# Kernel optimization log

Hardware: AMD Instinct MI355X
Metric: run time of the kernel (lower is better)

## Reference

```python
import jax, jax.numpy as jnp
import numpy as np

EPS = 1e-8


def setup_inputs() -> dict:
    key = jax.random.key(0)
    ks = jax.random.split(key, 4)
    B, Cin, Cout, K, S, H, W = 16, 256, 256, 3, 512, 128, 128
    return {
        "x": jax.random.normal(ks[0], (B, Cin, H, W), dtype=jnp.float32),
        "style": jax.random.normal(ks[1], (B, S), dtype=jnp.float32),
        "weight": jax.random.normal(ks[2], (1, Cout, Cin, K, K), dtype=jnp.float32),
        "mod_w": jax.random.normal(ks[3], (Cin, S), dtype=jnp.float32) * (1.0 / np.sqrt(S)),
        "mod_b": jnp.zeros((Cin,), dtype=jnp.float32),
        "bias": jnp.zeros((1, Cout, 1, 1), dtype=jnp.float32),
    }


def reference(x, style, weight, mod_w, mod_b, bias):
    B, Cin, H, W = x.shape
    _, Cout, _, K, _ = weight.shape
    scale = 1.0 / np.sqrt(Cin * K * K)

    # modulation: Linear(style_dim -> in_channel)
    s = style @ mod_w.T + mod_b                      # [B, Cin]
    w = scale * weight * s[:, None, :, None, None]   # [B, Cout, Cin, K, K]
    demod = jax.lax.rsqrt(jnp.sum(w * w, axis=(2, 3, 4)) + EPS)  # [B, Cout]
    w = w * demod[:, :, None, None, None]

    # grouped conv with groups = batch (per-sample weights)
    w = w.reshape(B * Cout, Cin, K, K)
    xg = x.reshape(1, B * Cin, H, W)
    out = jax.lax.conv_general_dilated(
        xg, w,
        window_strides=(1, 1),
        padding=[(1, 1), (1, 1)],
        dimension_numbers=("NCHW", "OIHW", "NCHW"),
        feature_group_count=B,
    )
    Ho, Wo = out.shape[2], out.shape[3]
    out = out.reshape(B, Cout, Ho, Wo)
    return out + bias
```

## Files before the change

### kernel.cpp

```cpp
#include <hip/hip_runtime.h>
#include <stdint.h>

typedef unsigned short u16;
typedef __attribute__((ext_vector_type(8))) short short8;
typedef __attribute__((ext_vector_type(4))) float f32x4;

#define AS1 __attribute__((address_space(1)))
#define AS3 __attribute__((address_space(3)))

static __device__ __forceinline__ void gload_lds16(const void* g, void* l) {
  __builtin_amdgcn_global_load_lds((const AS1 void*)g, (AS3 void*)l, 16, 0, 0);
}

static __device__ __forceinline__ u16 bf16r(float f) {
  union { float f; uint32_t u; } c; c.f = f;
  uint32_t u = c.u;
  u += 0x7fffu + ((u >> 16) & 1u);
  return (u16)(u >> 16);
}

static constexpr int NB = 16, CIN = 256, COUT = 256, HW = 128, SDIM = 512;
static constexpr float SCALE = 1.0f / 48.0f;

__global__ void k_style(const float* __restrict__ style, const float* __restrict__ mod_w,
                        const float* __restrict__ mod_b, float* __restrict__ s) {
  int b = blockIdx.x, ci = threadIdx.x;
  const float4* st = (const float4*)(style + (size_t)b * SDIM);
  const float4* mw = (const float4*)(mod_w + (size_t)ci * SDIM);
  float acc = 0.f;
  #pragma unroll 4
  for (int j = 0; j < SDIM / 4; ++j) {
    float4 a = st[j], w = mw[j];
    acc += a.x * w.x + a.y * w.y + a.z * w.z + a.w * w.w;
  }
  s[b * CIN + ci] = acc + mod_b[ci];
}

__global__ void k_wmod(const float* __restrict__ weight, const float* __restrict__ s,
                       u16* __restrict__ Wb) {
  __shared__ float wld[CIN * 9];
  __shared__ float red[8];
  int bid = blockIdx.x;
  int b = bid >> 8, co = bid & 255;
  int t = threadIdx.x;
  const float* wsrc = weight + (size_t)co * (CIN * 9);
  for (int i = t; i < CIN * 9; i += 256) wld[i] = wsrc[i];
  __syncthreads();
  int ci = t;
  float sv = s[b * CIN + ci];
  float v[9];
  float sq = 0.f;
  #pragma unroll
  for (int k = 0; k < 9; ++k) {
    float w = SCALE * wld[ci * 9 + k] * sv;
    v[k] = w;
    sq += w * w;
  }
  #pragma unroll
  for (int off = 32; off; off >>= 1) sq += __shfl_down(sq, off);
  int lane = t & 63, wid = t >> 6;
  if (lane == 0) red[wid] = sq;
  __syncthreads();
  if (t == 0) red[4] = rsqrtf(red[0] + red[1] + red[2] + red[3] + 1e-8f);
  __syncthreads();
  float demod = red[4];
  #pragma unroll
  for (int k = 0; k < 9; ++k) {
    Wb[(((size_t)b * 9 + k) * COUT + co) * CIN + ci] = bf16r(v[k] * demod);
  }
}

__global__ void k_xt(const float* __restrict__ x, u16* __restrict__ xTp) {
  __shared__ u16 T[128 * 65];
  int bid = blockIdx.x;
  int b = bid >> 7, h = bid & 127;
  int t = threadIdx.x;
  size_t rowbase = ((size_t)b * 130 + (h + 1)) * 130 * CIN;
  xTp[rowbase + t] = 0;
  xTp[rowbase + (size_t)129 * CIN + t] = 0;
  if (h == 0) {
    uint32_t* g = (uint32_t*)(xTp + (size_t)b * 130 * 130 * CIN);
    for (int i = t; i < 130 * CIN / 2; i += 256) g[i] = 0;
  }
  if (h == 127) {
    uint32_t* g = (uint32_t*)(xTp + ((size_t)b * 130 + 129) * 130 * CIN);
    for (int i = t; i < 130 * CIN / 2; i += 256) g[i] = 0;
  }
  for (int ci0 = 0; ci0 < CIN; ci0 += 64) {
    __syncthreads();
    #pragma unroll
    for (int i = 0; i < 8; ++i) {
      int idx = t + i * 256;
      int ci = idx >> 5, px4 = idx & 31;
      float4 v = *(const float4*)(x + (((size_t)b * CIN + ci0 + ci) * HW + h) * HW + px4 * 4);
      T[(px4 * 4 + 0) * 65 + ci] = bf16r(v.x);
      T[(px4 * 4 + 1) * 65 + ci] = bf16r(v.y);
      T[(px4 * 4 + 2) * 65 + ci] = bf16r(v.z);
      T[(px4 * 4 + 3) * 65 + ci] = bf16r(v.w);
    }
    __syncthreads();
    int ci = t & 63, pxo = t >> 6;
    #pragma unroll
    for (int i = 0; i < 32; ++i) {
      int px = i * 4 + pxo;
      xTp[rowbase + (size_t)(px + 1) * CIN + ci0 + ci] = T[px * 65 + ci];
    }
  }
}

static constexpr int SLOTU = 32768;

__global__ __launch_bounds__(512, 2) void k_conv(const u16* __restrict__ Wb,
                                                 const u16* __restrict__ xTp,
                                                 const float* __restrict__ bias,
                                                 float* __restrict__ out) {
  extern __shared__ u16 lds[];
  int bid = blockIdx.x;
  int swz = (bid & 7) * 128 + (bid >> 3);
  int b = swz >> 6, hp = swz & 63;
  int h0 = hp * 2;

  int t = threadIdx.x, lane = t & 63, wid = t >> 6;
  int wr = wid >> 2, wc = wid & 3;
  int rowoff = wid * 8 + (lane >> 3);
  int swzc = ((lane & 7) ^ (lane >> 3)) << 3;
  int cxor = (lane & 7) << 3;
  int klo = (lane >> 4) << 3;
  int arow = (wr * 128 + (lane & 15)) * 64;
  int brow = (wc * 64 + (lane & 15)) * 64;
  const size_t wbB = (size_t)b * 9 * 65536;
  const size_t xB = (size_t)b * 130 * 130 * 256;

  f32x4 acc[8][4];
  #pragma unroll
  for (int i = 0; i < 8; ++i)
    #pragma unroll
    for (int j = 0; j < 4; ++j) acc[i][j] = (f32x4)0.f;

  auto srcA = [&](int kta, int i) -> const u16* {
    int kpos = kta >> 2, ci0 = (kta & 3) << 6;
    return Wb + wbB + (size_t)kpos * 65536 + (size_t)(i * 64 + rowoff) * 256 + ci0 + swzc;
  };
  auto srcB = [&](int kta, int i) -> const u16* {
    int kpos = kta >> 2, ci0 = (kta & 3) << 6;
    int kh = kpos < 3 ? 0 : (kpos < 6 ? 1 : 2);
    int kw = kpos - kh * 3;
    int hh = h0 + kh + (i >> 1);
    int pxp = kw + (i & 1) * 64 + rowoff;
    return xTp + xB + ((size_t)hh * 130 + pxp) * 256 + ci0 + swzc;
  };

  {
    u16* A2 = lds;
    u16* B2 = lds + 16384;
    #pragma unroll
    for (int i = 0; i < 4; ++i) gload_lds16(srcA(0, i), A2 + (i * 64 + wid * 8) * 64);
    #pragma unroll
    for (int i = 0; i < 4; ++i) gload_lds16(srcB(0, i), B2 + (i * 64 + wid * 8) * 64);
  }
  __syncthreads();

  for (int kt = 0; kt < 36; ++kt) {
    u16* Ac = lds + (kt & 1) * SLOTU;
    u16* Bc = Ac + 16384;
    u16* An = lds + ((kt & 1) ^ 1) * SLOTU;
    u16* Bn = An + 16384;
    bool pf = kt < 35;
    int kta = kt + 1;

#define LD_A(M, KK) (*(const short8*)&Ac[arow + (M) * 1024 + (((KK) * 32 + klo) ^ cxor)])
#define LD_B(N, KK) (*(const short8*)&Bc[brow + (N) * 1024 + (((KK) * 32 + klo) ^ cxor)])

    short8 af0[8], bf0[4], af1[8], bf1[4];
    #pragma unroll
    for (int mt = 0; mt < 8; ++mt) af0[mt] = LD_A(mt, 0);
    #pragma unroll
    for (int nt = 0; nt < 4; ++nt) bf0[nt] = LD_B(nt, 0);
    if (pf) {
      #pragma unroll
      for (int i = 0; i < 4; ++i) gload_lds16(srcA(kta, i), An + (i * 64 + wid * 8) * 64);
    }
    #pragma unroll
    for (int nt = 0; nt < 4; ++nt) bf1[nt] = LD_B(nt, 1);
    #pragma unroll
    for (int mt = 0; mt < 8; ++mt)
      #pragma unroll
      for (int nt = 0; nt < 4; ++nt)
        acc[mt][nt] = __builtin_amdgcn_mfma_f32_16x16x32_bf16(af0[mt], bf0[nt], acc[mt][nt], 0, 0, 0);
    if (pf) {
      #pragma unroll
      for (int i = 0; i < 4; ++i) gload_lds16(srcB(kta, i), Bn + (i * 64 + wid * 8) * 64);
    }
    #pragma unroll
    for (int mt = 0; mt < 8; ++mt) af1[mt] = LD_A(mt, 1);
    #pragma unroll
    for (int mt = 0; mt < 8; ++mt)
      #pragma unroll
      for (int nt = 0; nt < 4; ++nt)
        acc[mt][nt] = __builtin_amdgcn_mfma_f32_16x16x32_bf16(af1[mt], bf1[nt], acc[mt][nt], 0, 0, 0);
    __syncthreads();
#undef LD_A
#undef LD_B
  }

  #pragma unroll
  for (int mt = 0; mt < 8; ++mt) {
    #pragma unroll
    for (int j = 0; j < 4; ++j) {
      int co = wr * 128 + mt * 16 + ((lane >> 4) * 4) + j;
      float bv = bias[co];
      #pragma unroll
      for (int nt = 0; nt < 4; ++nt) {
        int px = wc * 64 + nt * 16 + (lane & 15);
        int h = h0 + (px >> 7), w = px & 127;
        out[(((size_t)b * COUT + co) * HW + h) * HW + w] = acc[mt][nt][j] + bv;
      }
    }
  }
}

extern "C" void kernel_launch(void* const* d_in, const int* in_sizes, int n_in,
                              void* d_out, int out_size, void* d_ws, size_t ws_size,
                              hipStream_t stream) {
  const float* x      = (const float*)d_in[0];
  const float* style  = (const float*)d_in[1];
  const float* weight = (const float*)d_in[2];
  const float* mod_w  = (const float*)d_in[3];
  const float* mod_b  = (const float*)d_in[4];
  const float* bias   = (const float*)d_in[5];
  float* out = (float*)d_out;

  char* ws = (char*)d_ws;
  float* s   = (float*)ws;
  u16* Wb    = (u16*)(ws + 16384);
  u16* xTp   = (u16*)(ws + 16384 + (size_t)NB * 9 * COUT * CIN * 2);

  (void)hipFuncSetAttribute((const void*)k_conv,
                            hipFuncAttributeMaxDynamicSharedMemorySize, 2 * SLOTU * 2);

  k_style<<<NB, 256, 0, stream>>>(style, mod_w, mod_b, s);
  k_wmod<<<NB * COUT, 256, 0, stream>>>(weight, s, Wb);
  k_xt<<<NB * HW, 256, 0, stream>>>(x, xTp);
  k_conv<<<NB * (HW / 2), 512, 2 * SLOTU * 2, stream>>>(Wb, xTp, bias, out);
}
```

Baseline: 408.8 us.

## Restructure conv mainloop into fine-grained staged prefetch with split barriers and setprio

Rewrites the k_conv main loop so global-to-LDS loads for the next one and two k-steps are issued in smaller per-half-K chunks between MFMA phases. Explicit vmcnt waits and raw s_barriers replace the single __syncthreads per step. The LDS layout becomes 32-element-wide half-K slabs with a new XOR swizzle, and s_setprio raises priority around MFMA bursts. The aim is to overlap memory traffic with matrix math and cut LDS bank conflicts, at the cost of more barriers and a tricky wait-count schedule that could race if the counts are off.

```diff
diff --git a/kernel.cpp b/kernel.cpp
--- a/kernel.cpp
+++ b/kernel.cpp
@@ -122,12 +122,12 @@
 
   int t = threadIdx.x, lane = t & 63, wid = t >> 6;
   int wr = wid >> 2, wc = wid & 3;
-  int rowoff = wid * 8 + (lane >> 3);
-  int swzc = ((lane & 7) ^ (lane >> 3)) << 3;
-  int cxor = (lane & 7) << 3;
-  int klo = (lane >> 4) << 3;
-  int arow = (wr * 128 + (lane & 15)) * 64;
-  int brow = (wc * 64 + (lane & 15)) * 64;
+  int l15 = lane & 15;
+  int sa8 = (((lane >> 4) ^ ((lane >> 1) & 3))) * 8;
+  int aro = (wr * 128 + l15) * 32 + sa8;
+  int bro = 16384 + (wc * 64 + l15) * 32 + sa8;
+  int srow = t >> 2;
+  int ssrc8 = ((t & 3) ^ ((t >> 3) & 3)) * 8;
   const size_t wbB = (size_t)b * 9 * 65536;
   const size_t xB = (size_t)b * 130 * 130 * 256;
 
@@ -137,68 +137,99 @@
     #pragma unroll
     for (int j = 0; j < 4; ++j) acc[i][j] = (f32x4)0.f;
 
-  auto srcA = [&](int kta, int i) -> const u16* {
+  auto srcA = [&](int kta, int kk, int i) -> const u16* {
     int kpos = kta >> 2, ci0 = (kta & 3) << 6;
-    return Wb + wbB + (size_t)kpos * 65536 + (size_t)(i * 64 + rowoff) * 256 + ci0 + swzc;
+    return Wb + wbB + (size_t)kpos * 65536 + (size_t)(i * 128 + srow) * 256 + ci0 + kk * 32 + ssrc8;
   };
-  auto srcB = [&](int kta, int i) -> const u16* {
+  auto srcB = [&](int kta, int kk, int i) -> const u16* {
     int kpos = kta >> 2, ci0 = (kta & 3) << 6;
     int kh = kpos < 3 ? 0 : (kpos < 6 ? 1 : 2);
     int kw = kpos - kh * 3;
-    int hh = h0 + kh + (i >> 1);
-    int pxp = kw + (i & 1) * 64 + rowoff;
-    return xTp + xB + ((size_t)hh * 130 + pxp) * 256 + ci0 + swzc;
+    int hh = h0 + kh + i;
+    int pxp = kw + srow;
+    return xTp + xB + ((size_t)hh * 130 + pxp) * 256 + ci0 + kk * 32 + ssrc8;
   };
 
-  {
-    u16* A2 = lds;
-    u16* B2 = lds + 16384;
-    #pragma unroll
-    for (int i = 0; i < 4; ++i) gload_lds16(srcA(0, i), A2 + (i * 64 + wid * 8) * 64);
-    #pragma unroll
-    for (int i = 0; i < 4; ++i) gload_lds16(srcB(0, i), B2 + (i * 64 + wid * 8) * 64);
-  }
-  __syncthreads();
+#define STAGE_A(kta, kk)                                                                  \
+  do {                                                                                    \
+    u16* _d = lds + ((kta) & 1) * SLOTU + (kk) * 8192;                                    \
+    gload_lds16(srcA((kta), (kk), 0), _d + (wid * 16) * 32);                              \
+    gload_lds16(srcA((kta), (kk), 1), _d + (128 + wid * 16) * 32);                        \
+  } while (0)
+#define STAGE_B(kta, kk)                                                                  \
+  do {                                                                                    \
+    u16* _d = lds + ((kta) & 1) * SLOTU + 16384 + (kk) * 8192;                            \
+    gload_lds16(srcB((kta), (kk), 0), _d + (wid * 16) * 32);                              \
+    gload_lds16(srcB((kta), (kk), 1), _d + (128 + wid * 16) * 32);                        \
+  } while (0)
+#define BAR()                              \
+  asm volatile("" ::: "memory");           \
+  __builtin_amdgcn_s_barrier();            \
+  asm volatile("" ::: "memory");
+
+  STAGE_A(0, 0); STAGE_A(0, 1); STAGE_B(0, 0); STAGE_B(0, 1);
+  STAGE_A(1, 0); STAGE_A(1, 1); STAGE_B(1, 0);
+  asm volatile("s_waitcnt vmcnt(6)" ::: "memory");
+  BAR();
 
   for (int kt = 0; kt < 36; ++kt) {
-    u16* Ac = lds + (kt & 1) * SLOTU;
-    u16* Bc = Ac + 16384;
-    u16* An = lds + ((kt & 1) ^ 1) * SLOTU;
-    u16* Bn = An + 16384;
-    bool pf = kt < 35;
-    int kta = kt + 1;
-
-#define LD_A(M, KK) (*(const short8*)&Ac[arow + (M) * 1024 + (((KK) * 32 + klo) ^ cxor)])
-#define LD_B(N, KK) (*(const short8*)&Bc[brow + (N) * 1024 + (((KK) * 32 + klo) ^ cxor)])
-
-    short8 af0[8], bf0[4], af1[8], bf1[4];
-    #pragma unroll
-    for (int mt = 0; mt < 8; ++mt) af0[mt] = LD_A(mt, 0);
-    #pragma unroll
-    for (int nt = 0; nt < 4; ++nt) bf0[nt] = LD_B(nt, 0);
-    if (pf) {
-      #pragma unroll
-      for (int i = 0; i < 4; ++i) gload_lds16(srcA(kta, i), An + (i * 64 + wid * 8) * 64);
-    }
-    #pragma unroll
-    for (int nt = 0; nt < 4; ++nt) bf1[nt] = LD_B(nt, 1);
-    #pragma unroll
-    for (int mt = 0; mt < 8; ++mt)
-      #pragma unroll
-      for (int nt = 0; nt < 4; ++nt)
-        acc[mt][nt] = __builtin_amdgcn_mfma_f32_16x16x32_bf16(af0[mt], bf0[nt], acc[mt][nt], 0, 0, 0);
-    if (pf) {
-      #pragma unroll
-      for (int i = 0; i < 4; ++i) gload_lds16(srcB(kta, i), Bn + (i * 64 + wid * 8) * 64);
-    }
-    #pragma unroll
-    for (int mt = 0; mt < 8; ++mt) af1[mt] = LD_A(mt, 1);
-    #pragma unroll
-    for (int mt = 0; mt < 8; ++mt)
-      #pragma unroll
-      for (int nt = 0; nt < 4; ++nt)
-        acc[mt][nt] = __builtin_amdgcn_mfma_f32_16x16x32_bf16(af1[mt], bf1[nt], acc[mt][nt], 0, 0, 0);
-    __syncthreads();
+    const u16* S = lds + (kt & 1) * SLOTU;
+    bool pf1 = kt + 1 < 36, pf2 = kt + 2 < 36;
+
+#define LD_A(M, KK) (*(const short8*)&S[aro + (KK) * 8192 + (M) * 512])
+#define LD_B(N, KK) (*(const short8*)&S[bro + (KK) * 8192 + (N) * 512])
+
+    short8 a0[8], a1[8], bf[4];
+    #pragma unroll
+    for (int mt = 0; mt < 8; ++mt) a0[mt] = LD_A(mt, 0);
+    bf[0] = LD_B(0, 0); bf[1] = LD_B(1, 0);
+    if (pf1) STAGE_B(kt + 1, 1);
+    BAR();
+    __builtin_amdgcn_s_setprio(1);
+    #pragma unroll
+    for (int mt = 0; mt < 8; ++mt) {
+      acc[mt][0] = __builtin_amdgcn_mfma_f32_16x16x32_bf16(a0[mt], bf[0], acc[mt][0], 0, 0, 0);
+      acc[mt][1] = __builtin_amdgcn_mfma_f32_16x16x32_bf16(a0[mt], bf[1], acc[mt][1], 0, 0, 0);
+    }
+    __builtin_amdgcn_s_setprio(0);
+    BAR();
+    bf[2] = LD_B(2, 0); bf[3] = LD_B(3, 0);
+    #pragma unroll
+    for (int mt = 0; mt < 8; ++mt) a1[mt] = LD_A(mt, 1);
+    if (pf2) STAGE_A(kt + 2, 0);
+    BAR();
+    __builtin_amdgcn_s_setprio(1);
+    #pragma unroll
+    for (int mt = 0; mt < 8; ++mt) {
+      acc[mt][2] = __builtin_amdgcn_mfma_f32_16x16x32_bf16(a0[mt], bf[2], acc[mt][2], 0, 0, 0);
+      acc[mt][3] = __builtin_amdgcn_mfma_f32_16x16x32_bf16(a0[mt], bf[3], acc[mt][3], 0, 0, 0);
+    }
+    __builtin_amdgcn_s_setprio(0);
+    BAR();
+    bf[0] = LD_B(0, 1); bf[1] = LD_B(1, 1);
+    if (pf2) STAGE_A(kt + 2, 1);
+    BAR();
+    __builtin_amdgcn_s_setprio(1);
+    #pragma unroll
+    for (int mt = 0; mt < 8; ++mt) {
+      acc[mt][0] = __builtin_amdgcn_mfma_f32_16x16x32_bf16(a1[mt], bf[0], acc[mt][0], 0, 0, 0);
+      acc[mt][1] = __builtin_amdgcn_mfma_f32_16x16x32_bf16(a1[mt], bf[1], acc[mt][1], 0, 0, 0);
+    }
+    __builtin_amdgcn_s_setprio(0);
+    BAR();
+    bf[2] = LD_B(2, 1); bf[3] = LD_B(3, 1);
+    if (pf2) STAGE_B(kt + 2, 0);
+    BAR();
+    __builtin_amdgcn_s_setprio(1);
+    #pragma unroll
+    for (int mt = 0; mt < 8; ++mt) {
+      acc[mt][2] = __builtin_amdgcn_mfma_f32_16x16x32_bf16(a1[mt], bf[2], acc[mt][2], 0, 0, 0);
+      acc[mt][3] = __builtin_amdgcn_mfma_f32_16x16x32_bf16(a1[mt], bf[3], acc[mt][3], 0, 0, 0);
+    }
+    __builtin_amdgcn_s_setprio(0);
+    if (kt < 34)       asm volatile("s_waitcnt vmcnt(6)" ::: "memory");
+    else if (kt == 34) asm volatile("s_waitcnt vmcnt(0)" ::: "memory");
+    BAR();
 #undef LD_A
 #undef LD_B
   }
@@ -211,12 +242,15 @@
       float bv = bias[co];
       #pragma unroll
       for (int nt = 0; nt < 4; ++nt) {
-        int px = wc * 64 + nt * 16 + (lane & 15);
+        int px = wc * 64 + nt * 16 + l15;
         int h = h0 + (px >> 7), w = px & 127;
         out[(((size_t)b * COUT + co) * HW + h) * HW + w] = acc[mt][nt][j] + bv;
       }
     }
   }
+#undef STAGE_A
+#undef STAGE_B
+#undef BAR
 }
 
 extern "C" void kernel_launch(void* const* d_in, const int* in_sizes, int n_in,
```

After: 422.8 us. +3.4%, slower.

## Switch conv GEMM to 32x32x16 bf16 MFMA tiles and vectorize transpose stores

Applied to the files above, without the earlier changes.

The conv inner loop moves from 16x16x32 MFMA instructions to 32x32x16 ones. Each wave now holds 4x2 tiles of 32x32 accumulators, and the LDS fragment addressing and swizzle are rewritten to match, along with the epilogue output mapping. Larger MFMA tiles need fewer LDS fragment reads per FLOP and fewer instructions. The input transpose kernel also writes 16-byte short8 vectors instead of scalar u16 stores. The risks are LDS bank conflicts from the new access pattern and higher register pressure.

```diff
diff --git a/kernel.cpp b/kernel.cpp
--- a/kernel.cpp
+++ b/kernel.cpp
@@ -3,7 +3,7 @@
 
 typedef unsigned short u16;
 typedef __attribute__((ext_vector_type(8))) short short8;
-typedef __attribute__((ext_vector_type(4))) float f32x4;
+typedef __attribute__((ext_vector_type(16))) float f32x16;
 
 #define AS1 __attribute__((address_space(1)))
 #define AS3 __attribute__((address_space(3)))
@@ -86,6 +86,7 @@
     uint32_t* g = (uint32_t*)(xTp + ((size_t)b * 130 + 129) * 130 * CIN);
     for (int i = t; i < 130 * CIN / 2; i += 256) g[i] = 0;
   }
+  int c8 = t & 7, pxb = t >> 3;
   for (int ci0 = 0; ci0 < CIN; ci0 += 64) {
     __syncthreads();
     #pragma unroll
@@ -99,11 +100,13 @@
       T[(px4 * 4 + 3) * 65 + ci] = bf16r(v.w);
     }
     __syncthreads();
-    int ci = t & 63, pxo = t >> 6;
-    #pragma unroll
-    for (int i = 0; i < 32; ++i) {
-      int px = i * 4 + pxo;
-      xTp[rowbase + (size_t)(px + 1) * CIN + ci0 + ci] = T[px * 65 + ci];
+    #pragma unroll
+    for (int i = 0; i < 4; ++i) {
+      int px = i * 32 + pxb;
+      short8 v;
+      #pragma unroll
+      for (int j = 0; j < 8; ++j) v[j] = (short)T[px * 65 + c8 * 8 + j];
+      *(short8*)&xTp[rowbase + (size_t)(px + 1) * CIN + ci0 + c8 * 8] = v;
     }
   }
 }
@@ -122,20 +125,19 @@
 
   int t = threadIdx.x, lane = t & 63, wid = t >> 6;
   int wr = wid >> 2, wc = wid & 3;
+  int l31 = lane & 31, seg = lane >> 5, c7 = l31 & 7;
   int rowoff = wid * 8 + (lane >> 3);
   int swzc = ((lane & 7) ^ (lane >> 3)) << 3;
-  int cxor = (lane & 7) << 3;
-  int klo = (lane >> 4) << 3;
-  int arow = (wr * 128 + (lane & 15)) * 64;
-  int brow = (wc * 64 + (lane & 15)) * 64;
+  int aro = (wr * 128 + l31) * 64;
+  int bro = 16384 + (wc * 64 + l31) * 64;
   const size_t wbB = (size_t)b * 9 * 65536;
   const size_t xB = (size_t)b * 130 * 130 * 256;
 
-  f32x4 acc[8][4];
-  #pragma unroll
-  for (int i = 0; i < 8; ++i)
-    #pragma unroll
-    for (int j = 0; j < 4; ++j) acc[i][j] = (f32x4)0.f;
+  f32x16 acc[4][2];
+  #pragma unroll
+  for (int i = 0; i < 4; ++i)
+    #pragma unroll
+    for (int j = 0; j < 2; ++j) acc[i][j] = (f32x16)0.f;
 
   auto srcA = [&](int kta, int i) -> const u16* {
     int kpos = kta >> 2, ci0 = (kta & 3) << 6;
@@ -160,60 +162,71 @@
   }
   __syncthreads();
 
+  #pragma unroll 1
   for (int kt = 0; kt < 36; ++kt) {
-    u16* Ac = lds + (kt & 1) * SLOTU;
-    u16* Bc = Ac + 16384;
+    const u16* Ac = lds + (kt & 1) * SLOTU;
     u16* An = lds + ((kt & 1) ^ 1) * SLOTU;
     u16* Bn = An + 16384;
     bool pf = kt < 35;
     int kta = kt + 1;
 
-#define LD_A(M, KK) (*(const short8*)&Ac[arow + (M) * 1024 + (((KK) * 32 + klo) ^ cxor)])
-#define LD_B(N, KK) (*(const short8*)&Bc[brow + (N) * 1024 + (((KK) * 32 + klo) ^ cxor)])
-
-    short8 af0[8], bf0[4], af1[8], bf1[4];
-    #pragma unroll
-    for (int mt = 0; mt < 8; ++mt) af0[mt] = LD_A(mt, 0);
-    #pragma unroll
-    for (int nt = 0; nt < 4; ++nt) bf0[nt] = LD_B(nt, 0);
+#define CCOL(KS) ((((KS) * 2 + seg) ^ c7) << 3)
+#define LD_A(DST, KS)                                                            \
+    do {                                                                         \
+      _Pragma("unroll")                                                          \
+      for (int mt = 0; mt < 4; ++mt)                                             \
+        DST[mt] = *(const short8*)&Ac[aro + mt * 2048 + CCOL(KS)];               \
+    } while (0)
+#define LD_B(DST, KS)                                                            \
+    do {                                                                         \
+      _Pragma("unroll")                                                          \
+      for (int nt = 0; nt < 2; ++nt)                                             \
+        DST[nt] = *(const short8*)&Ac[bro + nt * 2048 + CCOL(KS)];               \
+    } while (0)
+#define MFMA8(SA, SB)                                                            \
+    _Pragma("unroll")                                                            \
+    for (int mt = 0; mt < 4; ++mt) {                                             \
+      acc[mt][0] = __builtin_amdgcn_mfma_f32_32x32x16_bf16(SA[mt], SB[0],        \
+                                                           acc[mt][0], 0, 0, 0); \
+      acc[mt][1] = __builtin_amdgcn_mfma_f32_32x32x16_bf16(SA[mt], SB[1],        \
+                                                           acc[mt][1], 0, 0, 0); \
+    }
+
+    short8 sA0[4], sA1[4], sA2[4], sA3[4], sB0[2], sB1[2], sB2[2], sB3[2];
+    LD_A(sA0, 0); LD_A(sA1, 1);
+    LD_B(sB0, 0);
     if (pf) {
       #pragma unroll
       for (int i = 0; i < 4; ++i) gload_lds16(srcA(kta, i), An + (i * 64 + wid * 8) * 64);
     }
-    #pragma unroll
-    for (int nt = 0; nt < 4; ++nt) bf1[nt] = LD_B(nt, 1);
-    #pragma unroll
-    for (int mt = 0; mt < 8; ++mt)
-      #pragma unroll
-      for (int nt = 0; nt < 4; ++nt)
-        acc[mt][nt] = __builtin_amdgcn_mfma_f32_16x16x32_bf16(af0[mt], bf0[nt], acc[mt][nt], 0, 0, 0);
+    LD_B(sB1, 1);
+    MFMA8(sA0, sB0);
+    MFMA8(sA1, sB1);
     if (pf) {
       #pragma unroll
       for (int i = 0; i < 4; ++i) gload_lds16(srcB(kta, i), Bn + (i * 64 + wid * 8) * 64);
     }
-    #pragma unroll
-    for (int mt = 0; mt < 8; ++mt) af1[mt] = LD_A(mt, 1);
-    #pragma unroll
-    for (int mt = 0; mt < 8; ++mt)
-      #pragma unroll
-      for (int nt = 0; nt < 4; ++nt)
-        acc[mt][nt] = __builtin_amdgcn_mfma_f32_16x16x32_bf16(af1[mt], bf1[nt], acc[mt][nt], 0, 0, 0);
+    LD_A(sA2, 2); LD_A(sA3, 3);
+    LD_B(sB2, 2); LD_B(sB3, 3);
+    MFMA8(sA2, sB2);
+    MFMA8(sA3, sB3);
     __syncthreads();
+#undef CCOL
 #undef LD_A
 #undef LD_B
-  }
-
-  #pragma unroll
-  for (int mt = 0; mt < 8; ++mt) {
-    #pragma unroll
-    for (int j = 0; j < 4; ++j) {
-      int co = wr * 128 + mt * 16 + ((lane >> 4) * 4) + j;
-      float bv = bias[co];
-      #pragma unroll
-      for (int nt = 0; nt < 4; ++nt) {
-        int px = wc * 64 + nt * 16 + (lane & 15);
-        int h = h0 + (px >> 7), w = px & 127;
-        out[(((size_t)b * COUT + co) * HW + h) * HW + w] = acc[mt][nt][j] + bv;
+#undef MFMA8
+  }
+
+  #pragma unroll
+  for (int mt = 0; mt < 4; ++mt) {
+    #pragma unroll
+    for (int nt = 0; nt < 2; ++nt) {
+      int px = wc * 64 + nt * 32 + l31;
+      int h = h0 + (px >> 7), w = px & 127;
+      #pragma unroll
+      for (int j = 0; j < 16; ++j) {
+        int co = wr * 128 + mt * 32 + (j & 3) + 8 * (j >> 2) + 4 * seg;
+        out[(((size_t)b * COUT + co) * HW + h) * HW + w] = acc[mt][nt][j] + bias[co];
       }
     }
   }
```

After: 435.7 us. 1.07x slower.
